# Performance work log

Measured on AMD Instinct MI355X. Metric: run time of the kernel, lower is better.

The kernel has to match this reference:

```python
import jax, jax.numpy as jnp
import numpy as np

DIM = 1024
N_HEAD = 16
HEAD_DIM = DIM // N_HEAD
B, T = 4, 2048
NEG = -1e9


def setup_inputs() -> dict:
    key = jax.random.key(0)
    ks = jax.random.split(key, 5)
    x = jax.random.normal(ks[0], (B, T, DIM), dtype=jnp.float32)
    # additive causal mask, broadcast over batch and heads
    causal = jnp.triu(jnp.full((T, T), NEG, dtype=jnp.float32), k=1)
    mask = causal[None, None, :, :]  # [1,1,T,T]
    s = 1.0 / np.sqrt(DIM)
    wq = jax.random.normal(ks[1], (DIM, DIM), dtype=jnp.float32) * s
    wk = jax.random.normal(ks[2], (DIM, DIM), dtype=jnp.float32) * s
    wv = jax.random.normal(ks[3], (DIM, DIM), dtype=jnp.float32) * s
    wo = jax.random.normal(ks[4], (DIM, DIM), dtype=jnp.float32) * s
    return {"x": x, "mask": mask, "wq": wq, "wk": wk, "wv": wv, "wo": wo}


def reference(x, mask, wq, wk, wv, wo):
    Bn, Tn, C = x.shape
    # torch nn.Linear(dim,dim,bias=False): y = x @ W^T
    q = (x @ wq.T).reshape(Bn, Tn, N_HEAD, HEAD_DIM).transpose(0, 2, 1, 3)  # [B,H,T,D]
    k = (x @ wk.T).reshape(Bn, Tn, N_HEAD, HEAD_DIM).transpose(0, 2, 1, 3)
    v = (x @ wv.T).reshape(Bn, Tn, N_HEAD, HEAD_DIM).transpose(0, 2, 1, 3)
    scale = 1.0 / np.sqrt(HEAD_DIM).astype(np.float32)
    attn = jnp.einsum('bhqd,bhkd->bhqk', q, k) * scale  # [B,H,T,T]
    attn = attn + mask
    attn = jax.nn.softmax(attn, axis=-1)
    out = jnp.einsum('bhqk,bhkd->bhqd', attn, v)  # [B,H,T,D]
    out = out.transpose(0, 2, 1, 3).reshape(Bn, Tn, C)
    return out @ wo.T
```

## Files before the change

### kernel.cpp

```cpp
#include <hip/hip_runtime.h>
#include <hip/hip_bf16.h>

typedef __attribute__((ext_vector_type(8))) short short8;
typedef __attribute__((ext_vector_type(4))) short short4v;
typedef __attribute__((ext_vector_type(4))) float float4v;

#define DIM   1024
#define NH    16
#define HD    64
#define BSZ   4
#define TSZ   2048
#define BT    (BSZ*TSZ)

#define SBIAS 24.0f

#define PIDX(row, col) ((((row)*64 + (col)) ^ (((row)&7) << 3)))

typedef const __attribute__((address_space(1))) void* gptr_t;
typedef __attribute__((address_space(3))) void* lptr_t;

__device__ __forceinline__ short f2bs(float x) {
    __hip_bfloat16 h = __float2bfloat16(x);
    return __builtin_bit_cast(short, h);
}

__global__ __launch_bounds__(256) void cvt_kernel(
    const float* __restrict__ x,  const float* __restrict__ wq,
    const float* __restrict__ wk, const float* __restrict__ wv,
    const float* __restrict__ wo,
    __hip_bfloat16* __restrict__ xb,  __hip_bfloat16* __restrict__ wqb,
    __hip_bfloat16* __restrict__ wkb, __hip_bfloat16* __restrict__ wvb,
    __hip_bfloat16* __restrict__ wob)
{
    int bid = blockIdx.x;
    const float* src; __hip_bfloat16* dst; int base;
    if (bid < 8192) { src = x; dst = xb; base = bid; }
    else {
        int wsel = (bid - 8192) >> 10;
        base = (bid - 8192) & 1023;
        src = (wsel == 0) ? wq : (wsel == 1) ? wk : (wsel == 2) ? wv : wo;
        dst = (wsel == 0) ? wqb : (wsel == 1) ? wkb : (wsel == 2) ? wvb : wob;
    }
    size_t off = (size_t)base * 1024 + threadIdx.x * 4;
    float4v v = *(const float4v*)(src + off);
    short4v o;
    o[0] = f2bs(v[0]); o[1] = f2bs(v[1]); o[2] = f2bs(v[2]); o[3] = f2bs(v[3]);
    *(short4v*)((short*)dst + off) = o;
}

__device__ __forceinline__ void gemm_core(
    const __hip_bfloat16* __restrict__ A,
    const __hip_bfloat16* __restrict__ B,
    __hip_bfloat16* smA, __hip_bfloat16* smB,
    int m0, int n0, int tid, float4v acc[4][4])
{
    const int wid = tid >> 6, lane = tid & 63;
    const int quad = lane >> 4, l15 = lane & 15;
    const int l7 = l15 & 7;
    const int wm = (wid >> 1) * 64, wn = (wid & 1) * 64;
    const int srow = tid >> 3;
    const int scol = ((tid & 7) ^ (srow & 7)) * 8;

    const __hip_bfloat16* gA0 = A + (size_t)(m0 + srow) * DIM + scol;
    const __hip_bfloat16* gB0 = B + (size_t)(n0 + srow) * DIM + scol;

    for (int kc = 0; kc < DIM; kc += 64) {
        __syncthreads();
#pragma unroll
        for (int j = 0; j < 4; j++) {
            __builtin_amdgcn_global_load_lds((gptr_t)(gA0 + (size_t)(j*32)*DIM + kc),
                (lptr_t)(smA + j*2048 + tid*8), 16, 0, 0);
            __builtin_amdgcn_global_load_lds((gptr_t)(gB0 + (size_t)(j*32)*DIM + kc),
                (lptr_t)(smB + j*2048 + tid*8), 16, 0, 0);
        }
        __syncthreads();

#pragma unroll
        for (int s = 0; s < 2; s++) {
            short8 a[4], b[4];
#pragma unroll
            for (int mb = 0; mb < 4; mb++)
                a[mb] = *(const short8*)(smA + (wm + mb*16 + l15)*64 + ((s*4 + quad) ^ l7)*8);
#pragma unroll
            for (int nb = 0; nb < 4; nb++)
                b[nb] = *(const short8*)(smB + (wn + nb*16 + l15)*64 + ((s*4 + quad) ^ l7)*8);
#pragma unroll
            for (int mb = 0; mb < 4; mb++)
#pragma unroll
                for (int nb = 0; nb < 4; nb++)
                    acc[mb][nb] = __builtin_amdgcn_mfma_f32_16x16x32_bf16(
                        a[mb], b[nb], acc[mb][nb], 0, 0, 0);
        }
    }
}

__global__ __launch_bounds__(256) void qkv_gemm(
    const __hip_bfloat16* __restrict__ xb,
    const __hip_bfloat16* __restrict__ wqb,
    const __hip_bfloat16* __restrict__ wkb,
    const __hip_bfloat16* __restrict__ wvb,
    __hip_bfloat16* __restrict__ Qt,
    __hip_bfloat16* __restrict__ Kb,
    __hip_bfloat16* __restrict__ Vt)
{
    __shared__ __hip_bfloat16 smA[128*64];
    __shared__ __hip_bfloat16 smB[128*64];

    const int z = blockIdx.z;
    const __hip_bfloat16* w = (z == 0) ? wqb : ((z == 1) ? wkb : wvb);
    const int tid = threadIdx.x;
    const int wid = tid >> 6, lane = tid & 63;
    const int quad = lane >> 4, l15 = lane & 15;
    const int m0 = blockIdx.x * 128, n0 = blockIdx.y * 128;
    const int wm0 = m0 + (wid >> 1) * 64;
    const int wn0 = n0 + (wid & 1) * 64;
    const float qscale = 0.1803368801111204f;

    float4v acc[4][4];
#pragma unroll
    for (int i = 0; i < 4; i++)
#pragma unroll
        for (int j = 0; j < 4; j++)
#pragma unroll
            for (int r = 0; r < 4; r++) acc[i][j][r] = 0.0f;

    gemm_core(xb, w, smA, smB, m0, n0, tid, acc);

    if (z != 1) {
        __hip_bfloat16* dst = (z == 0) ? Qt : Vt;
        const float sc = (z == 0) ? qscale : 1.0f;
        const int h = wn0 >> 6;
#pragma unroll
        for (int mb = 0; mb < 4; mb++) {
            int m = wm0 + mb*16 + quad*4;
            int bb = m >> 11, t0 = m & 2047;
#pragma unroll
            for (int nb = 0; nb < 4; nb++) {
                int d = nb*16 + l15;
                short4v pk;
                pk[0] = f2bs(acc[mb][nb][0] * sc); pk[1] = f2bs(acc[mb][nb][1] * sc);
                pk[2] = f2bs(acc[mb][nb][2] * sc); pk[3] = f2bs(acc[mb][nb][3] * sc);
                *(short4v*)(dst + (size_t)((bb*NH + h)*HD + d)*TSZ + t0) = pk;
            }
        }
    } else {
#pragma unroll
        for (int mb = 0; mb < 4; mb++)
#pragma unroll
            for (int r = 0; r < 4; r++) {
                int m = wm0 + mb*16 + quad*4 + r;
                int bb = m >> 11, t = m & 2047;
#pragma unroll
                for (int nb = 0; nb < 4; nb++) {
                    int n = wn0 + nb*16 + l15;
                    int h = n >> 6, d = n & 63;
                    Kb[(size_t)((bb*NH + h)*TSZ + t)*HD + d] =
                        __float2bfloat16(acc[mb][nb][r]);
                }
            }
    }
}

__global__ __launch_bounds__(256, 2) void attn(
    const __hip_bfloat16* __restrict__ Qt,
    const __hip_bfloat16* __restrict__ Kb,
    const __hip_bfloat16* __restrict__ Vt,
    __hip_bfloat16* __restrict__ Ob)
{
    __shared__ __hip_bfloat16 smK[64*64];
    __shared__ __hip_bfloat16 smV[64*64];
    __shared__ __hip_bfloat16 Pl[4][32*64];

    const int qperm[16] = {15,14,13,12,8,9,10,11,4,5,6,7,3,2,1,0};
    const int bh = blockIdx.x;
    const int qt = qperm[blockIdx.y];
    const int q0 = qt * 128;
    const int tid = threadIdx.x;
    const int wid = tid >> 6, lane = tid & 63;
    const int quad = lane >> 4, l15 = lane & 15;
    const int l7 = l15 & 7;
    const int q0w = q0 + wid * 32;

    const __hip_bfloat16* Qp = Qt + (size_t)bh * HD * TSZ;
    const __hip_bfloat16* Kp = Kb + (size_t)bh * TSZ * HD;
    const __hip_bfloat16* Vp = Vt + (size_t)bh * HD * TSZ;
    __hip_bfloat16* P = &Pl[wid][0];

    const int srow = tid >> 3;
    const int scol = ((tid & 7) ^ (srow & 7)) * 8;

    short8 bq[2][2];
#pragma unroll
    for (int nt = 0; nt < 2; nt++)
#pragma unroll
        for (int c = 0; c < 2; c++) {
            short8 v;
#pragma unroll
            for (int j = 0; j < 8; j++)
                v[j] = ((const short*)Qp)[(size_t)(c*32 + quad*8 + j)*TSZ
                                          + (q0w + nt*16 + l15)];
            bq[nt][c] = v;
        }

    float lsum[2] = {0.f, 0.f};
    float4v ot[4][2];
#pragma unroll
    for (int mt = 0; mt < 4; mt++)
#pragma unroll
        for (int nt = 0; nt < 2; nt++)
#pragma unroll
            for (int r = 0; r < 4; r++) ot[mt][nt][r] = 0.f;

    const int ntb = 2*qt + 2;
    for (int it = 0; it < ntb; ++it) {
        const int k0 = it * 64;

        __syncthreads();
#pragma unroll
        for (int c = 0; c < 2; c++) {
            __builtin_amdgcn_global_load_lds(
                (gptr_t)(Kp + (size_t)(k0 + srow + 32*c)*HD + scol),
                (lptr_t)(smK + tid*8 + c*2048), 16, 0, 0);
            __builtin_amdgcn_global_load_lds(
                (gptr_t)(Vp + (size_t)(srow + 32*c)*TSZ + k0 + scol),
                (lptr_t)(smV + tid*8 + c*2048), 16, 0, 0);
        }
        __syncthreads();

        if (k0 > q0w + 31) continue;

        float4v st[4][2];
#pragma unroll
        for (int mt = 0; mt < 4; mt++)
#pragma unroll
            for (int nt = 0; nt < 2; nt++)
#pragma unroll
                for (int r = 0; r < 4; r++) st[mt][nt][r] = -SBIAS;
#pragma unroll
        for (int c = 0; c < 2; c++)
#pragma unroll
            for (int mt = 0; mt < 4; mt++) {
                short8 ak = *(const short8*)(smK + (mt*16 + l15)*64 + ((c*4 + quad) ^ l7)*8);
                st[mt][0] = __builtin_amdgcn_mfma_f32_16x16x32_bf16(ak, bq[0][c], st[mt][0], 0, 0, 0);
                st[mt][1] = __builtin_amdgcn_mfma_f32_16x16x32_bf16(ak, bq[1][c], st[mt][1], 0, 0, 0);
            }

        if (k0 + 63 > q0w) {
#pragma unroll
            for (int mt = 0; mt < 4; mt++) {
                if (k0 + mt*16 + 15 > q0w) {
#pragma unroll
                    for (int nt = 0; nt < 2; nt++) {
                        int qn = q0w + nt*16 + l15;
#pragma unroll
                        for (int r = 0; r < 4; r++) {
                            int kg = k0 + mt*16 + quad*4 + r;
                            if (kg > qn) st[mt][nt][r] = -1e30f;
                        }
                    }
                }
            }
        }

#pragma unroll
        for (int nt = 0; nt < 2; nt++) {
            float rs = 0.f;
#pragma unroll
            for (int mt = 0; mt < 4; mt++) {
                float p0 = exp2f(st[mt][nt][0]);
                float p1 = exp2f(st[mt][nt][1]);
                float p2 = exp2f(st[mt][nt][2]);
                float p3 = exp2f(st[mt][nt][3]);
                rs += (p0 + p1) + (p2 + p3);
                short4v pk;
                pk[0] = f2bs(p0); pk[1] = f2bs(p1);
                pk[2] = f2bs(p2); pk[3] = f2bs(p3);
                *(short4v*)(P + PIDX(nt*16 + l15, mt*16 + quad*4)) = pk;
            }
            lsum[nt] += rs;
        }

        short8 bp[2][2];
#pragma unroll
        for (int nt = 0; nt < 2; nt++)
#pragma unroll
            for (int c2 = 0; c2 < 2; c2++)
                bp[nt][c2] = *(const short8*)(P + PIDX(nt*16 + l15, c2*32 + quad*8));

#pragma unroll
        for (int c2 = 0; c2 < 2; c2++)
#pragma unroll
            for (int mt = 0; mt < 4; mt++) {
                short8 av = *(const short8*)(smV + (mt*16 + l15)*64 + ((c2*4 + quad) ^ l7)*8);
                ot[mt][0] = __builtin_amdgcn_mfma_f32_16x16x32_bf16(av, bp[0][c2], ot[mt][0], 0, 0, 0);
                ot[mt][1] = __builtin_amdgcn_mfma_f32_16x16x32_bf16(av, bp[1][c2], ot[mt][1], 0, 0, 0);
            }
    }

    const int b = bh >> 4, h = bh & 15;
#pragma unroll
    for (int nt = 0; nt < 2; nt++) {
        float ls = lsum[nt];
        ls += __shfl_xor(ls, 16);
        ls += __shfl_xor(ls, 32);
        const float inv = 1.0f / ls;
        const int qn = q0w + nt*16 + l15;
        const size_t rowbase = (size_t)((b*TSZ + qn)*NH + h) * HD;
#pragma unroll
        for (int mt = 0; mt < 4; mt++) {
            short4v pk;
            pk[0] = f2bs(ot[mt][nt][0] * inv); pk[1] = f2bs(ot[mt][nt][1] * inv);
            pk[2] = f2bs(ot[mt][nt][2] * inv); pk[3] = f2bs(ot[mt][nt][3] * inv);
            *(short4v*)(Ob + rowbase + mt*16 + quad*4) = pk;
        }
    }
}

__global__ __launch_bounds__(256) void out_gemm(
    const __hip_bfloat16* __restrict__ A,
    const __hip_bfloat16* __restrict__ w,
    float* __restrict__ out)
{
    __shared__ __hip_bfloat16 smA[2][128*64];
    __shared__ __hip_bfloat16 smB[2][128*64];

    const int tid = threadIdx.x;
    const int wid = tid >> 6, lane = tid & 63;
    const int quad = lane >> 4, l15 = lane & 15;
    const int l7 = l15 & 7;
    const int m0 = blockIdx.x * 128, n0 = blockIdx.y * 128;
    const int wm = (wid >> 1) * 64, wn = (wid & 1) * 64;
    const int wm0 = m0 + wm, wn0 = n0 + wn;
    const int srow = tid >> 3;
    const int scol = ((tid & 7) ^ (srow & 7)) * 8;

    const __hip_bfloat16* gA0 = A + (size_t)(m0 + srow) * DIM + scol;
    const __hip_bfloat16* gB0 = w + (size_t)(n0 + srow) * DIM + scol;

    float4v acc[4][4];
#pragma unroll
    for (int i = 0; i < 4; i++)
#pragma unroll
        for (int j = 0; j < 4; j++)
#pragma unroll
            for (int r = 0; r < 4; r++) acc[i][j][r] = 0.0f;

#pragma unroll
    for (int j = 0; j < 4; j++) {
        __builtin_amdgcn_global_load_lds((gptr_t)(gA0 + (size_t)(j*32)*DIM),
            (lptr_t)(&smA[0][0] + j*2048 + tid*8), 16, 0, 0);
        __builtin_amdgcn_global_load_lds((gptr_t)(gB0 + (size_t)(j*32)*DIM),
            (lptr_t)(&smB[0][0] + j*2048 + tid*8), 16, 0, 0);
    }

    int cur = 0;
    for (int kc = 0; kc < DIM; kc += 64) {
        __syncthreads();

        if (kc + 64 < DIM) {
            const int kn = kc + 64;
#pragma unroll
            for (int j = 0; j < 4; j++) {
                __builtin_amdgcn_global_load_lds((gptr_t)(gA0 + (size_t)(j*32)*DIM + kn),
                    (lptr_t)(&smA[cur^1][0] + j*2048 + tid*8), 16, 0, 0);
                __builtin_amdgcn_global_load_lds((gptr_t)(gB0 + (size_t)(j*32)*DIM + kn),
                    (lptr_t)(&smB[cur^1][0] + j*2048 + tid*8), 16, 0, 0);
            }
        }

        const __hip_bfloat16* sA = &smA[cur][0];
        const __hip_bfloat16* sB = &smB[cur][0];
#pragma unroll
        for (int s = 0; s < 2; s++) {
            short8 a[4], b[4];
#pragma unroll
            for (int mb = 0; mb < 4; mb++)
                a[mb] = *(const short8*)(sA + (wm + mb*16 + l15)*64 + ((s*4 + quad) ^ l7)*8);
#pragma unroll
            for (int nb = 0; nb < 4; nb++)
                b[nb] = *(const short8*)(sB + (wn + nb*16 + l15)*64 + ((s*4 + quad) ^ l7)*8);
#pragma unroll
            for (int mb = 0; mb < 4; mb++)
#pragma unroll
                for (int nb = 0; nb < 4; nb++)
                    acc[mb][nb] = __builtin_amdgcn_mfma_f32_16x16x32_bf16(
                        a[mb], b[nb], acc[mb][nb], 0, 0, 0);
        }
        cur ^= 1;
    }

#pragma unroll
    for (int mb = 0; mb < 4; mb++)
#pragma unroll
        for (int nb = 0; nb < 4; nb++)
#pragma unroll
            for (int r = 0; r < 4; r++) {
                int m = wm0 + mb*16 + quad*4 + r;
                int n = wn0 + nb*16 + l15;
                out[(size_t)m*DIM + n] = acc[mb][nb][r];
            }
}

extern "C" void kernel_launch(void* const* d_in, const int* in_sizes, int n_in,
                              void* d_out, int out_size, void* d_ws, size_t ws_size,
                              hipStream_t stream) {
    const float* x  = (const float*)d_in[0];
    const float* wq = (const float*)d_in[2];
    const float* wk = (const float*)d_in[3];
    const float* wv = (const float*)d_in[4];
    const float* wo = (const float*)d_in[5];
    float* out = (float*)d_out;

    char* ws = (char*)d_ws;
    const size_t MB = (size_t)1024 * 1024;
    __hip_bfloat16* Qt  = (__hip_bfloat16*)(ws);
    __hip_bfloat16* Kb  = (__hip_bfloat16*)(ws + 16*MB);
    __hip_bfloat16* Vt  = (__hip_bfloat16*)(ws + 32*MB);
    __hip_bfloat16* xb  = (__hip_bfloat16*)(ws + 48*MB);
    __hip_bfloat16* Ob  = (__hip_bfloat16*)(ws + 48*MB);
    __hip_bfloat16* wqb = (__hip_bfloat16*)(ws + 64*MB);
    __hip_bfloat16* wkb = (__hip_bfloat16*)(ws + 66*MB);
    __hip_bfloat16* wvb = (__hip_bfloat16*)(ws + 68*MB);
    __hip_bfloat16* wob = (__hip_bfloat16*)(ws + 70*MB);

    dim3 blk(256);
    cvt_kernel<<<dim3(8192 + 4*1024), blk, 0, stream>>>(
        x, wq, wk, wv, wo, xb, wqb, wkb, wvb, wob);
    qkv_gemm<<<dim3(BT/128, DIM/128, 3), blk, 0, stream>>>(
        xb, wqb, wkb, wvb, Qt, Kb, Vt);
    attn<<<dim3(BSZ*NH, 16), blk, 0, stream>>>(Qt, Kb, Vt, Ob);
    out_gemm<<<dim3(BT/128, DIM/128), blk, 0, stream>>>(Ob, wob, out);
}
```

Baseline: 249.6 us.

## Fuse Q/K/V projections into one GEMM block sharing the x tile

Each QKV GEMM block now loads one x tile into LDS and multiplies it against all three weight tiles (Q, K, V), accumulating three 64x64 per-wave results. The z grid dimension is removed, so there are a third as many blocks and x is read from global memory once instead of three times. In exchange, accumulator registers triple (192 floats per thread) and LDS per block doubles. Combined with the new launch bound of 2 blocks/CU, this risks spills and lower occupancy, and the grid may be too small to fill all CUs.

```diff
diff --git a/kernel.cpp b/kernel.cpp
--- a/kernel.cpp
+++ b/kernel.cpp
@@ -48,53 +48,7 @@
     *(short4v*)((short*)dst + off) = o;
 }
 
-__device__ __forceinline__ void gemm_core(
-    const __hip_bfloat16* __restrict__ A,
-    const __hip_bfloat16* __restrict__ B,
-    __hip_bfloat16* smA, __hip_bfloat16* smB,
-    int m0, int n0, int tid, float4v acc[4][4])
-{
-    const int wid = tid >> 6, lane = tid & 63;
-    const int quad = lane >> 4, l15 = lane & 15;
-    const int l7 = l15 & 7;
-    const int wm = (wid >> 1) * 64, wn = (wid & 1) * 64;
-    const int srow = tid >> 3;
-    const int scol = ((tid & 7) ^ (srow & 7)) * 8;
-
-    const __hip_bfloat16* gA0 = A + (size_t)(m0 + srow) * DIM + scol;
-    const __hip_bfloat16* gB0 = B + (size_t)(n0 + srow) * DIM + scol;
-
-    for (int kc = 0; kc < DIM; kc += 64) {
-        __syncthreads();
-#pragma unroll
-        for (int j = 0; j < 4; j++) {
-            __builtin_amdgcn_global_load_lds((gptr_t)(gA0 + (size_t)(j*32)*DIM + kc),
-                (lptr_t)(smA + j*2048 + tid*8), 16, 0, 0);
-            __builtin_amdgcn_global_load_lds((gptr_t)(gB0 + (size_t)(j*32)*DIM + kc),
-                (lptr_t)(smB + j*2048 + tid*8), 16, 0, 0);
-        }
-        __syncthreads();
-
-#pragma unroll
-        for (int s = 0; s < 2; s++) {
-            short8 a[4], b[4];
-#pragma unroll
-            for (int mb = 0; mb < 4; mb++)
-                a[mb] = *(const short8*)(smA + (wm + mb*16 + l15)*64 + ((s*4 + quad) ^ l7)*8);
-#pragma unroll
-            for (int nb = 0; nb < 4; nb++)
-                b[nb] = *(const short8*)(smB + (wn + nb*16 + l15)*64 + ((s*4 + quad) ^ l7)*8);
-#pragma unroll
-            for (int mb = 0; mb < 4; mb++)
-#pragma unroll
-                for (int nb = 0; nb < 4; nb++)
-                    acc[mb][nb] = __builtin_amdgcn_mfma_f32_16x16x32_bf16(
-                        a[mb], b[nb], acc[mb][nb], 0, 0, 0);
-        }
-    }
-}
-
-__global__ __launch_bounds__(256) void qkv_gemm(
+__global__ __launch_bounds__(256, 2) void qkv_gemm(
     const __hip_bfloat16* __restrict__ xb,
     const __hip_bfloat16* __restrict__ wqb,
     const __hip_bfloat16* __restrict__ wkb,
@@ -104,31 +58,72 @@
     __hip_bfloat16* __restrict__ Vt)
 {
     __shared__ __hip_bfloat16 smA[128*64];
-    __shared__ __hip_bfloat16 smB[128*64];
-
-    const int z = blockIdx.z;
-    const __hip_bfloat16* w = (z == 0) ? wqb : ((z == 1) ? wkb : wvb);
+    __shared__ __hip_bfloat16 smB[3][128*64];
+
     const int tid = threadIdx.x;
     const int wid = tid >> 6, lane = tid & 63;
     const int quad = lane >> 4, l15 = lane & 15;
+    const int l7 = l15 & 7;
     const int m0 = blockIdx.x * 128, n0 = blockIdx.y * 128;
-    const int wm0 = m0 + (wid >> 1) * 64;
-    const int wn0 = n0 + (wid & 1) * 64;
+    const int wm = (wid >> 1) * 64, wn = (wid & 1) * 64;
+    const int wm0 = m0 + wm, wn0 = n0 + wn;
+    const int srow = tid >> 3;
+    const int scol = ((tid & 7) ^ (srow & 7)) * 8;
     const float qscale = 0.1803368801111204f;
 
-    float4v acc[4][4];
-#pragma unroll
-    for (int i = 0; i < 4; i++)
-#pragma unroll
-        for (int j = 0; j < 4; j++)
-#pragma unroll
-            for (int r = 0; r < 4; r++) acc[i][j][r] = 0.0f;
-
-    gemm_core(xb, w, smA, smB, m0, n0, tid, acc);
-
-    if (z != 1) {
-        __hip_bfloat16* dst = (z == 0) ? Qt : Vt;
-        const float sc = (z == 0) ? qscale : 1.0f;
+    const __hip_bfloat16* gA0 = xb  + (size_t)(m0 + srow) * DIM + scol;
+    const __hip_bfloat16* gBq = wqb + (size_t)(n0 + srow) * DIM + scol;
+    const __hip_bfloat16* gBk = wkb + (size_t)(n0 + srow) * DIM + scol;
+    const __hip_bfloat16* gBv = wvb + (size_t)(n0 + srow) * DIM + scol;
+
+    float4v acc[3][4][4];
+#pragma unroll
+    for (int z = 0; z < 3; z++)
+#pragma unroll
+        for (int i = 0; i < 4; i++)
+#pragma unroll
+            for (int j = 0; j < 4; j++)
+#pragma unroll
+                for (int r = 0; r < 4; r++) acc[z][i][j][r] = 0.0f;
+
+    for (int kc = 0; kc < DIM; kc += 64) {
+        __syncthreads();
+#pragma unroll
+        for (int j = 0; j < 4; j++) {
+            __builtin_amdgcn_global_load_lds((gptr_t)(gA0 + (size_t)(j*32)*DIM + kc),
+                (lptr_t)(smA + j*2048 + tid*8), 16, 0, 0);
+            __builtin_amdgcn_global_load_lds((gptr_t)(gBq + (size_t)(j*32)*DIM + kc),
+                (lptr_t)(&smB[0][0] + j*2048 + tid*8), 16, 0, 0);
+            __builtin_amdgcn_global_load_lds((gptr_t)(gBk + (size_t)(j*32)*DIM + kc),
+                (lptr_t)(&smB[1][0] + j*2048 + tid*8), 16, 0, 0);
+            __builtin_amdgcn_global_load_lds((gptr_t)(gBv + (size_t)(j*32)*DIM + kc),
+                (lptr_t)(&smB[2][0] + j*2048 + tid*8), 16, 0, 0);
+        }
+        __syncthreads();
+
+#pragma unroll
+        for (int s = 0; s < 2; s++) {
+            short8 a[4];
+#pragma unroll
+            for (int mb = 0; mb < 4; mb++)
+                a[mb] = *(const short8*)(smA + (wm + mb*16 + l15)*64 + ((s*4 + quad) ^ l7)*8);
+#pragma unroll
+            for (int z = 0; z < 3; z++) {
+                short8 b[4];
+#pragma unroll
+                for (int nb = 0; nb < 4; nb++)
+                    b[nb] = *(const short8*)(&smB[z][0] + (wn + nb*16 + l15)*64 + ((s*4 + quad) ^ l7)*8);
+#pragma unroll
+                for (int mb = 0; mb < 4; mb++)
+#pragma unroll
+                    for (int nb = 0; nb < 4; nb++)
+                        acc[z][mb][nb] = __builtin_amdgcn_mfma_f32_16x16x32_bf16(
+                            a[mb], b[nb], acc[z][mb][nb], 0, 0, 0);
+            }
+        }
+    }
+
+    {
         const int h = wn0 >> 6;
 #pragma unroll
         for (int mb = 0; mb < 4; mb++) {
@@ -137,28 +132,31 @@
 #pragma unroll
             for (int nb = 0; nb < 4; nb++) {
                 int d = nb*16 + l15;
-                short4v pk;
-                pk[0] = f2bs(acc[mb][nb][0] * sc); pk[1] = f2bs(acc[mb][nb][1] * sc);
-                pk[2] = f2bs(acc[mb][nb][2] * sc); pk[3] = f2bs(acc[mb][nb][3] * sc);
-                *(short4v*)(dst + (size_t)((bb*NH + h)*HD + d)*TSZ + t0) = pk;
-            }
-        }
-    } else {
-#pragma unroll
-        for (int mb = 0; mb < 4; mb++)
-#pragma unroll
-            for (int r = 0; r < 4; r++) {
-                int m = wm0 + mb*16 + quad*4 + r;
-                int bb = m >> 11, t = m & 2047;
-#pragma unroll
-                for (int nb = 0; nb < 4; nb++) {
-                    int n = wn0 + nb*16 + l15;
-                    int h = n >> 6, d = n & 63;
-                    Kb[(size_t)((bb*NH + h)*TSZ + t)*HD + d] =
-                        __float2bfloat16(acc[mb][nb][r]);
-                }
-            }
-    }
+                short4v pq, pv;
+                pq[0] = f2bs(acc[0][mb][nb][0] * qscale); pq[1] = f2bs(acc[0][mb][nb][1] * qscale);
+                pq[2] = f2bs(acc[0][mb][nb][2] * qscale); pq[3] = f2bs(acc[0][mb][nb][3] * qscale);
+                pv[0] = f2bs(acc[2][mb][nb][0]); pv[1] = f2bs(acc[2][mb][nb][1]);
+                pv[2] = f2bs(acc[2][mb][nb][2]); pv[3] = f2bs(acc[2][mb][nb][3]);
+                size_t base = (size_t)((bb*NH + h)*HD + d)*TSZ + t0;
+                *(short4v*)(Qt + base) = pq;
+                *(short4v*)(Vt + base) = pv;
+            }
+        }
+    }
+#pragma unroll
+    for (int mb = 0; mb < 4; mb++)
+#pragma unroll
+        for (int r = 0; r < 4; r++) {
+            int m = wm0 + mb*16 + quad*4 + r;
+            int bb = m >> 11, t = m & 2047;
+#pragma unroll
+            for (int nb = 0; nb < 4; nb++) {
+                int n = wn0 + nb*16 + l15;
+                int h = n >> 6, d = n & 63;
+                Kb[(size_t)((bb*NH + h)*TSZ + t)*HD + d] =
+                    __float2bfloat16(acc[1][mb][nb][r]);
+            }
+        }
 }
 
 __global__ __launch_bounds__(256, 2) void attn(
@@ -426,7 +424,7 @@
     dim3 blk(256);
     cvt_kernel<<<dim3(8192 + 4*1024), blk, 0, stream>>>(
         x, wq, wk, wv, wo, xb, wqb, wkb, wvb, wob);
-    qkv_gemm<<<dim3(BT/128, DIM/128, 3), blk, 0, stream>>>(
+    qkv_gemm<<<dim3(BT/128, DIM/128), blk, 0, stream>>>(
         xb, wqb, wkb, wvb, Qt, Kb, Vt);
     attn<<<dim3(BSZ*NH, 16), blk, 0, stream>>>(Qt, Kb, Vt, Ob);
     out_gemm<<<dim3(BT/128, DIM/128), blk, 0, stream>>>(Ob, wob, out);
```

Result: no change. 246.6 us (-1.2%).
